# Kernel tuning notes

Hardware: AMD Instinct MI355X
Metric: run time of the kernel (lower is better)

The kernel has to match this reference:

```python
import jax, jax.numpy as jnp
import numpy as np

N_NODES = 25000
N_EDGES = 250000
DIM = 64
HEADS = 4
BN_EPS = 1e-5


def setup_inputs() -> dict:
    key = jax.random.key(0)
    ks = jax.random.split(key, 6)
    x = jax.random.normal(ks[0], (N_NODES, DIM), dtype=jnp.float32)
    edge_index = jax.random.randint(ks[1], (2, N_EDGES), 0, N_NODES)
    edge_attr = jax.random.normal(ks[2], (N_EDGES, DIM), dtype=jnp.float32)
    # learned params of GATGNN_AGAT_LAYER (xavier-ish scale)
    W = jax.random.normal(ks[3], (2 * DIM, HEADS * DIM), dtype=jnp.float32) * 0.05
    att = jax.random.normal(ks[4], (1, HEADS, 2 * DIM), dtype=jnp.float32) * 0.05
    bias = jnp.zeros((DIM,), dtype=jnp.float32)
    # BatchNorm1d(heads) in eval mode (running stats)
    bn_gamma = jnp.ones((HEADS,), dtype=jnp.float32)
    bn_beta = jnp.zeros((HEADS,), dtype=jnp.float32)
    bn_mean = jnp.zeros((HEADS,), dtype=jnp.float32)
    bn_var = jnp.ones((HEADS,), dtype=jnp.float32)
    return {"x": x, "edge_attr": edge_attr, "W": W, "att": att, "bias": bias,
            "bn_gamma": bn_gamma, "bn_beta": bn_beta, "bn_mean": bn_mean,
            "bn_var": bn_var, "edge_index": edge_index}


def reference(x, edge_attr, W, att, bias, bn_gamma, bn_beta, bn_mean, bn_var, edge_index):
    act = jax.nn.softplus  # act='softplus' in DSDCrystal
    # flow='target_to_source': i = edge_index[0] (aggregation index), j = edge_index[1]
    idx_i = edge_index[0]
    idx_j = edge_index[1]
    x_i = x[idx_i]                                   # [E, D] gather
    x_j = x[idx_j]                                   # [E, D] gather
    out_i = act(jnp.concatenate([x_i, edge_attr], axis=-1) @ W)  # [E, H*D]
    out_j = act(jnp.concatenate([x_j, edge_attr], axis=-1) @ W)  # [E, H*D]
    out_i = out_i.reshape(-1, HEADS, DIM)            # [E, H, D]
    out_j = out_j.reshape(-1, HEADS, DIM)
    # multi-head attention logits
    alpha = act(jnp.sum(jnp.concatenate([out_i, out_j], axis=-1) * att, axis=-1))  # [E, H]
    # BatchNorm1d(heads), eval mode
    alpha = act((alpha - bn_mean) / jnp.sqrt(bn_var + BN_EPS) * bn_gamma + bn_beta)
    # segment softmax over edges sharing the same target node i
    amax = jax.ops.segment_max(alpha, idx_i, num_segments=N_NODES)  # [N, H]
    e = jnp.exp(alpha - amax[idx_i])
    denom = jax.ops.segment_sum(e, idx_i, num_segments=N_NODES)[idx_i]  # [E, H]
    alpha = e / denom
    # weighted messages, scatter-add aggregation (dropout p=0.0 / eval)
    msg = out_j * alpha[:, :, None]                  # [E, H, D]
    aggr = jax.ops.segment_sum(msg, idx_i, num_segments=N_NODES)  # [N, H, D]
    # update: mean over heads + bias
    return aggr.mean(axis=1) + bias                  # [N, D]
```

## Files before the change

### kernel.cpp

```cpp
#include <hip/hip_runtime.h>
#include <hip/hip_bf16.h>
#include <math.h>

#define NN 25000
#define NE 250000
#define DD 64
#define HH 4
#define NGROUP (NE / 16)
#define NB 98

typedef __attribute__((ext_vector_type(8))) short bf16x8;
typedef __attribute__((ext_vector_type(4))) float f32x4;

#define WT_LD 136

__device__ __forceinline__ float softplus_f(float x) {
    return fmaxf(x, 0.0f) + __logf(1.0f + __expf(-fabsf(x)));
}

__device__ __forceinline__ unsigned short f2bf(float f) {
    __hip_bfloat16 h = __float2bfloat16(f);
    unsigned short u;
    __builtin_memcpy(&u, &h, 2);
    return u;
}

__device__ __forceinline__ float bf2f(unsigned short u) {
    return __uint_as_float(((unsigned int)u) << 16);
}

__device__ __forceinline__ unsigned int cvtpk(float a, float b) {
    unsigned int r;
    asm("v_cvt_pk_bf16_f32 %0, %1, %2" : "=v"(r) : "v"(a), "v"(b));
    return r;
}

__device__ __forceinline__ void load8(const float* p, bf16x8& hi, bf16x8& lo) {
    float4 a = *(const float4*)p;
    float4 b = *(const float4*)(p + 4);
    float v[8] = {a.x, a.y, a.z, a.w, b.x, b.y, b.z, b.w};
#pragma unroll
    for (int i = 0; i < 8; ++i) {
        unsigned short h = f2bf(v[i]);
        hi[i] = (short)h;
        lo[i] = (short)f2bf(v[i] - bf2f(h));
    }
}

__global__ __launch_bounds__(512, 2)
void k_edge(const float* __restrict__ x, const float* __restrict__ ea,
            const float* __restrict__ W, const float* __restrict__ att,
            const float* __restrict__ bn_g, const float* __restrict__ bn_b,
            const float* __restrict__ bn_m, const float* __restrict__ bn_v,
            const int* __restrict__ eidx, const int* __restrict__ slot,
            unsigned short* __restrict__ outj,
            float* __restrict__ expa)
{
    __shared__ unsigned short Wsh[256 * WT_LD];
    __shared__ float attI[256], attJ[256];

    const int tid = threadIdx.x;
    const int lane = tid & 63;
    const int q = lane >> 4;
    const int r = lane & 15;

    float bnsc[HH], bnsh[HH];
#pragma unroll
    for (int t = 0; t < HH; ++t) {
        float inv = rsqrtf(bn_v[t] + 1e-5f);
        bnsc[t] = bn_g[t] * inv;
        bnsh[t] = bn_b[t] - bn_m[t] * bn_g[t] * inv;
    }

    for (int idx = tid; idx < 32768; idx += 512) {
        int k = idx >> 8, n = idx & 255;
        Wsh[n * WT_LD + k] = f2bf(W[idx]);
    }
    if (tid < 256) {
        int c = tid;
        float sc = bnsc[c >> 6];
        attI[c] = att[(c >> 6) * 128 + (c & 63)] * sc;
        attJ[c] = att[(c >> 6) * 128 + 64 + (c & 63)] * sc;
    }
    __syncthreads();

    const int gw = blockIdx.x * 8 + (tid >> 6);
    const int nw = gridDim.x * 8;

    for (int g = gw; g < NGROUP; g += nw) {
        const int e0 = g * 16;
        const int ei = eidx[e0 + r];
        const int ej = eidx[NE + e0 + r];
        const float* xi = x + (size_t)ei * DD;
        const float* xj = x + (size_t)ej * DD;
        const float* ev = ea + (size_t)(e0 + r) * DD;

        int sl[4];
#pragma unroll
        for (int reg = 0; reg < 4; ++reg) sl[reg] = slot[e0 + q * 4 + reg];

        bf16x8 Ahi[6], Alo[6];
        load8(xi + q * 8,      Ahi[0], Alo[0]);
        load8(xi + 32 + q * 8, Ahi[1], Alo[1]);
        load8(xj + q * 8,      Ahi[2], Alo[2]);
        load8(xj + 32 + q * 8, Ahi[3], Alo[3]);
        load8(ev + q * 8,      Ahi[4], Alo[4]);
        load8(ev + 32 + q * 8, Ahi[5], Alo[5]);

        float lg[4][4];
#pragma unroll
        for (int a = 0; a < 4; ++a)
#pragma unroll
            for (int b = 0; b < 4; ++b) lg[a][b] = 0.f;

#pragma unroll
        for (int nt = 0; nt < 4; ++nt) {
            f32x4 ai[4], aj[4];
#pragma unroll
            for (int h = 0; h < 4; ++h) {
                ai[h] = (f32x4){0.f, 0.f, 0.f, 0.f};
                aj[h] = (f32x4){0.f, 0.f, 0.f, 0.f};
            }
#pragma unroll
            for (int h = 0; h < 4; ++h) {
                const unsigned short* bp = &Wsh[((nt + 4 * h) * 16 + r) * WT_LD + q * 8];
#pragma unroll
                for (int kt = 0; kt < 4; ++kt) {
                    bf16x8 bf = *(const bf16x8*)(bp + kt * 32);
                    const int fi = (kt < 2) ? kt : kt + 2;
                    const int fj = kt + 2;
                    ai[h] = __builtin_amdgcn_mfma_f32_16x16x32_bf16(Ahi[fi], bf, ai[h], 0, 0, 0);
                    ai[h] = __builtin_amdgcn_mfma_f32_16x16x32_bf16(Alo[fi], bf, ai[h], 0, 0, 0);
                    aj[h] = __builtin_amdgcn_mfma_f32_16x16x32_bf16(Ahi[fj], bf, aj[h], 0, 0, 0);
                    aj[h] = __builtin_amdgcn_mfma_f32_16x16x32_bf16(Alo[fj], bf, aj[h], 0, 0, 0);
                }
            }
            const int dbase = nt * 16 + r;
#pragma unroll
            for (int reg = 0; reg < 4; ++reg) {
                float sp[4];
#pragma unroll
                for (int h = 0; h < 4; ++h) {
                    const int c = dbase + 64 * h;
                    float spi = softplus_f(ai[h][reg]);
                    float spj = softplus_f(aj[h][reg]);
                    lg[reg][h] += spi * attI[c] + spj * attJ[c];
                    sp[h] = spj;
                }
                uint2 pk;
                pk.x = cvtpk(sp[0], sp[1]);
                pk.y = cvtpk(sp[2], sp[3]);
                *(uint2*)&outj[(size_t)(unsigned)sl[reg] * 256 + dbase * 4] = pk;
            }
        }

#pragma unroll
        for (int off = 1; off < 16; off <<= 1) {
#pragma unroll
            for (int a = 0; a < 4; ++a)
#pragma unroll
                for (int b = 0; b < 4; ++b)
                    lg[a][b] += __shfl_xor(lg[a][b], off, 64);
        }
        float exv[4][4];
#pragma unroll
        for (int reg = 0; reg < 4; ++reg)
#pragma unroll
            for (int h = 0; h < 4; ++h)
                exv[reg][h] = 1.0f + __expf(lg[reg][h] + bnsh[h]);

        if (r < 4) {
#pragma unroll
            for (int reg = 0; reg < 4; ++reg)
                expa[sl[reg] * 4 + r] = exv[reg][r];
        }
    }
}

__global__ __launch_bounds__(256)
void k_hist(const int* __restrict__ eidx, int* __restrict__ deg)
{
    const int e = blockIdx.x * 256 + threadIdx.x;
    if (e < NE) atomicAdd(&deg[eidx[e]], 1);
}

__global__ __launch_bounds__(256)
void k_scanA(const int* __restrict__ deg, int* __restrict__ bsum)
{
    __shared__ int sh[256];
    const int t = threadIdx.x;
    const int idx = blockIdx.x * 256 + t;
    sh[t] = (idx < NN) ? deg[idx] : 0;
    __syncthreads();
#pragma unroll
    for (int off = 128; off >= 1; off >>= 1) {
        if (t < off) sh[t] += sh[t + off];
        __syncthreads();
    }
    if (t == 0) bsum[blockIdx.x] = sh[0];
}

__global__ __launch_bounds__(128)
void k_scanB(const int* __restrict__ bsum, int* __restrict__ boff)
{
    __shared__ int sh[128];
    const int t = threadIdx.x;
    const int v = (t < NB) ? bsum[t] : 0;
    sh[t] = v;
    __syncthreads();
#pragma unroll
    for (int off = 1; off < 128; off <<= 1) {
        int u = (t >= off) ? sh[t - off] : 0;
        __syncthreads();
        sh[t] += u;
        __syncthreads();
    }
    if (t < NB) boff[t] = sh[t] - v;
}

__global__ __launch_bounds__(256)
void k_scanC(const int* __restrict__ deg, const int* __restrict__ boff,
             int* __restrict__ offs)
{
    __shared__ int sh[256];
    const int t = threadIdx.x;
    const int idx = blockIdx.x * 256 + t;
    const int v = (idx < NN) ? deg[idx] : 0;
    sh[t] = v;
    __syncthreads();
#pragma unroll
    for (int off = 1; off < 256; off <<= 1) {
        int u = (t >= off) ? sh[t - off] : 0;
        __syncthreads();
        sh[t] += u;
        __syncthreads();
    }
    if (idx < NN) offs[idx] = boff[blockIdx.x] + sh[t] - v;
    if (idx == NN - 1) offs[NN] = boff[blockIdx.x] + sh[t];
}

__global__ __launch_bounds__(256)
void k_fill(const int* __restrict__ eidx, const int* __restrict__ offs,
            int* __restrict__ cursor, int* __restrict__ slot)
{
    const int e = blockIdx.x * 256 + threadIdx.x;
    if (e < NE) {
        const int i = eidx[e];
        const int p = atomicAdd(&cursor[i], 1);
        slot[e] = offs[i] + p;
    }
}

__global__ __launch_bounds__(256)
void k_aggr(const int* __restrict__ offs,
            const unsigned short* __restrict__ outj,
            const float* __restrict__ expa,
            const float* __restrict__ bias, float* __restrict__ out)
{
    const int n = blockIdx.x * 4 + (threadIdx.x >> 6);
    const int lane = threadIdx.x & 63;
    const int beg = offs[n];
    const int end = offs[n + 1];

    float a0 = 0.f, a1 = 0.f, a2 = 0.f, a3 = 0.f;
    float d0 = 0.f, d1 = 0.f, d2 = 0.f, d3 = 0.f;
    int t = beg;
    for (; t + 4 <= end; t += 4) {
        float4 x0 = *(const float4*)&expa[(size_t)t * 4];
        float4 x1 = *(const float4*)&expa[(size_t)(t + 1) * 4];
        float4 x2 = *(const float4*)&expa[(size_t)(t + 2) * 4];
        float4 x3 = *(const float4*)&expa[(size_t)(t + 3) * 4];
        ushort4 v0 = *(const ushort4*)&outj[((size_t)t << 8) | (lane << 2)];
        ushort4 v1 = *(const ushort4*)&outj[((size_t)(t + 1) << 8) | (lane << 2)];
        ushort4 v2 = *(const ushort4*)&outj[((size_t)(t + 2) << 8) | (lane << 2)];
        ushort4 v3 = *(const ushort4*)&outj[((size_t)(t + 3) << 8) | (lane << 2)];
        a0 += x0.x * bf2f(v0.x); a1 += x0.y * bf2f(v0.y);
        a2 += x0.z * bf2f(v0.z); a3 += x0.w * bf2f(v0.w);
        d0 += x0.x; d1 += x0.y; d2 += x0.z; d3 += x0.w;
        a0 += x1.x * bf2f(v1.x); a1 += x1.y * bf2f(v1.y);
        a2 += x1.z * bf2f(v1.z); a3 += x1.w * bf2f(v1.w);
        d0 += x1.x; d1 += x1.y; d2 += x1.z; d3 += x1.w;
        a0 += x2.x * bf2f(v2.x); a1 += x2.y * bf2f(v2.y);
        a2 += x2.z * bf2f(v2.z); a3 += x2.w * bf2f(v2.w);
        d0 += x2.x; d1 += x2.y; d2 += x2.z; d3 += x2.w;
        a0 += x3.x * bf2f(v3.x); a1 += x3.y * bf2f(v3.y);
        a2 += x3.z * bf2f(v3.z); a3 += x3.w * bf2f(v3.w);
        d0 += x3.x; d1 += x3.y; d2 += x3.z; d3 += x3.w;
    }
    for (; t < end; ++t) {
        float4 xv = *(const float4*)&expa[(size_t)t * 4];
        ushort4 v = *(const ushort4*)&outj[((size_t)t << 8) | (lane << 2)];
        a0 += xv.x * bf2f(v.x); a1 += xv.y * bf2f(v.y);
        a2 += xv.z * bf2f(v.z); a3 += xv.w * bf2f(v.w);
        d0 += xv.x; d1 += xv.y; d2 += xv.z; d3 += xv.w;
    }
    float rsum = 0.f;
    if (end > beg)
        rsum = 0.25f * (a0 / d0 + a1 / d1 + a2 / d2 + a3 / d3);
    out[n * DD + lane] = rsum + bias[lane];
}

extern "C" void kernel_launch(void* const* d_in, const int* in_sizes, int n_in,
                              void* d_out, int out_size, void* d_ws, size_t ws_size,
                              hipStream_t stream)
{
    (void)in_sizes; (void)n_in; (void)out_size; (void)ws_size;
    const float* x    = (const float*)d_in[0];
    const float* ea   = (const float*)d_in[1];
    const float* W    = (const float*)d_in[2];
    const float* att  = (const float*)d_in[3];
    const float* bias = (const float*)d_in[4];
    const float* bn_g = (const float*)d_in[5];
    const float* bn_b = (const float*)d_in[6];
    const float* bn_m = (const float*)d_in[7];
    const float* bn_v = (const float*)d_in[8];
    const int*   eidx = (const int*)d_in[9];
    float* out = (float*)d_out;

    char* ws = (char*)d_ws;
    unsigned short* outj = (unsigned short*)ws;
    float* expa   = (float*)(ws + 128000000ull);
    int*   deg    = (int*)(ws + 132000000ull);
    int*   cursor = (int*)(ws + 132100000ull);
    int*   offs   = (int*)(ws + 132200000ull);
    int*   slot   = (int*)(ws + 132300032ull);
    int*   bsum   = (int*)(ws + 133300032ull);
    int*   boff   = (int*)(ws + 133300544ull);

    hipMemsetAsync(deg, 0, 200000, stream);

    k_hist<<<dim3((NE + 255) / 256), dim3(256), 0, stream>>>(eidx, deg);
    k_scanA<<<dim3(NB), dim3(256), 0, stream>>>(deg, bsum);
    k_scanB<<<dim3(1), dim3(128), 0, stream>>>(bsum, boff);
    k_scanC<<<dim3(NB), dim3(256), 0, stream>>>(deg, boff, offs);
    k_fill<<<dim3((NE + 255) / 256), dim3(256), 0, stream>>>(eidx, offs, cursor, slot);
    k_edge<<<dim3(512), dim3(512), 0, stream>>>(
        x, ea, W, att, bn_g, bn_b, bn_m, bn_v, eidx, slot, outj, expa);
    k_aggr<<<dim3(NN / 4), dim3(256), 0, stream>>>(offs, outj, expa, bias, out);
}
```

Measured before the change: 343.1 us.

## Fuse CSR build into one cooperative kernel with grid syncs

The memset, histogram, three scan stages and slot-fill kernels are merged into one cooperative kernel that uses grid-wide barriers between phases. This removes several kernel launches and their inter-kernel gaps from the preprocessing stage. Separately, the bf16 packing of the out_j values moves from an inline-asm packed convert to per-element conversion through the HIP intrinsic. That second change may add a few instructions in the edge kernel. The cooperative launch needs all 98 blocks to be resident at the same time and adds grid-sync overhead; the histogram and fill loops now stride over about 25k threads instead of one thread per edge.

```diff
diff --git a/kernel.cpp b/kernel.cpp
--- a/kernel.cpp
+++ b/kernel.cpp
@@ -1,6 +1,9 @@
 #include <hip/hip_runtime.h>
 #include <hip/hip_bf16.h>
+#include <hip/hip_cooperative_groups.h>
 #include <math.h>
+
+namespace cg = cooperative_groups;
 
 #define NN 25000
 #define NE 250000
@@ -27,12 +30,6 @@
 
 __device__ __forceinline__ float bf2f(unsigned short u) {
     return __uint_as_float(((unsigned int)u) << 16);
-}
-
-__device__ __forceinline__ unsigned int cvtpk(float a, float b) {
-    unsigned int r;
-    asm("v_cvt_pk_bf16_f32 %0, %1, %2" : "=v"(r) : "v"(a), "v"(b));
-    return r;
 }
 
 __device__ __forceinline__ void load8(const float* p, bf16x8& hi, bf16x8& lo) {
@@ -138,19 +135,17 @@
             const int dbase = nt * 16 + r;
 #pragma unroll
             for (int reg = 0; reg < 4; ++reg) {
-                float sp[4];
+                ushort4 pk;
+                unsigned short* pkp = (unsigned short*)&pk;
 #pragma unroll
                 for (int h = 0; h < 4; ++h) {
                     const int c = dbase + 64 * h;
                     float spi = softplus_f(ai[h][reg]);
                     float spj = softplus_f(aj[h][reg]);
                     lg[reg][h] += spi * attI[c] + spj * attJ[c];
-                    sp[h] = spj;
+                    pkp[h] = f2bf(spj);
                 }
-                uint2 pk;
-                pk.x = cvtpk(sp[0], sp[1]);
-                pk.y = cvtpk(sp[2], sp[3]);
-                *(uint2*)&outj[(size_t)(unsigned)sl[reg] * 256 + dbase * 4] = pk;
+                *(ushort4*)&outj[(size_t)(unsigned)sl[reg] * 256 + dbase * 4] = pk;
             }
         }
 
@@ -178,18 +173,20 @@
 }
 
 __global__ __launch_bounds__(256)
-void k_hist(const int* __restrict__ eidx, int* __restrict__ deg)
+void k_csr(const int* __restrict__ eidx, int* __restrict__ deg,
+           int* __restrict__ cursor, int* __restrict__ offs,
+           int* __restrict__ slot, int* __restrict__ bsum)
 {
-    const int e = blockIdx.x * 256 + threadIdx.x;
-    if (e < NE) atomicAdd(&deg[eidx[e]], 1);
-}
-
-__global__ __launch_bounds__(256)
-void k_scanA(const int* __restrict__ deg, int* __restrict__ bsum)
-{
+    cg::grid_group grid = cg::this_grid();
     __shared__ int sh[256];
     const int t = threadIdx.x;
     const int idx = blockIdx.x * 256 + t;
+    const int GSZ = gridDim.x * 256;
+
+    for (int i = idx; i < NN; i += GSZ) { deg[i] = 0; cursor[i] = 0; }
+    grid.sync();
+    for (int e = idx; e < NE; e += GSZ) atomicAdd(&deg[eidx[e]], 1);
+    grid.sync();
     sh[t] = (idx < NN) ? deg[idx] : 0;
     __syncthreads();
 #pragma unroll
@@ -198,33 +195,21 @@
         __syncthreads();
     }
     if (t == 0) bsum[blockIdx.x] = sh[0];
-}
-
-__global__ __launch_bounds__(128)
-void k_scanB(const int* __restrict__ bsum, int* __restrict__ boff)
-{
-    __shared__ int sh[128];
-    const int t = threadIdx.x;
-    const int v = (t < NB) ? bsum[t] : 0;
-    sh[t] = v;
-    __syncthreads();
-#pragma unroll
-    for (int off = 1; off < 128; off <<= 1) {
-        int u = (t >= off) ? sh[t - off] : 0;
+    grid.sync();
+    if (blockIdx.x == 0) {
+        int v = (t < NB) ? bsum[t] : 0;
+        sh[t] = v;
         __syncthreads();
-        sh[t] += u;
-        __syncthreads();
-    }
-    if (t < NB) boff[t] = sh[t] - v;
-}
-
-__global__ __launch_bounds__(256)
-void k_scanC(const int* __restrict__ deg, const int* __restrict__ boff,
-             int* __restrict__ offs)
-{
-    __shared__ int sh[256];
-    const int t = threadIdx.x;
-    const int idx = blockIdx.x * 256 + t;
+#pragma unroll
+        for (int off = 1; off < 256; off <<= 1) {
+            int u = (t >= off) ? sh[t - off] : 0;
+            __syncthreads();
+            sh[t] += u;
+            __syncthreads();
+        }
+        if (t < NB) bsum[t] = sh[t] - v;
+    }
+    grid.sync();
     const int v = (idx < NN) ? deg[idx] : 0;
     sh[t] = v;
     __syncthreads();
@@ -235,16 +220,10 @@
         sh[t] += u;
         __syncthreads();
     }
-    if (idx < NN) offs[idx] = boff[blockIdx.x] + sh[t] - v;
-    if (idx == NN - 1) offs[NN] = boff[blockIdx.x] + sh[t];
-}
-
-__global__ __launch_bounds__(256)
-void k_fill(const int* __restrict__ eidx, const int* __restrict__ offs,
-            int* __restrict__ cursor, int* __restrict__ slot)
-{
-    const int e = blockIdx.x * 256 + threadIdx.x;
-    if (e < NE) {
+    if (idx < NN) offs[idx] = bsum[blockIdx.x] + sh[t] - v;
+    if (idx == NN - 1) offs[NN] = bsum[blockIdx.x] + sh[t];
+    grid.sync();
+    for (int e = idx; e < NE; e += GSZ) {
         const int i = eidx[e];
         const int p = atomicAdd(&cursor[i], 1);
         slot[e] = offs[i] + p;
@@ -325,15 +304,11 @@
     int*   offs   = (int*)(ws + 132200000ull);
     int*   slot   = (int*)(ws + 132300032ull);
     int*   bsum   = (int*)(ws + 133300032ull);
-    int*   boff   = (int*)(ws + 133300544ull);
-
-    hipMemsetAsync(deg, 0, 200000, stream);
-
-    k_hist<<<dim3((NE + 255) / 256), dim3(256), 0, stream>>>(eidx, deg);
-    k_scanA<<<dim3(NB), dim3(256), 0, stream>>>(deg, bsum);
-    k_scanB<<<dim3(1), dim3(128), 0, stream>>>(bsum, boff);
-    k_scanC<<<dim3(NB), dim3(256), 0, stream>>>(deg, boff, offs);
-    k_fill<<<dim3((NE + 255) / 256), dim3(256), 0, stream>>>(eidx, offs, cursor, slot);
+
+    void* csr_args[] = {(void*)&eidx, (void*)&deg, (void*)&cursor,
+                        (void*)&offs, (void*)&slot, (void*)&bsum};
+    hipLaunchCooperativeKernel((void*)k_csr, dim3(NB), dim3(256),
+                               csr_args, 0, stream);
     k_edge<<<dim3(512), dim3(512), 0, stream>>>(
         x, ea, W, att, bn_g, bn_b, bn_m, bn_v, eidx, slot, outj, expa);
     k_aggr<<<dim3(NN / 4), dim3(256), 0, stream>>>(offs, outj, expa, bias, out);
```

Result: slower. 385.6 us (+12.4%).
